# Kernel optimization log

Hardware: AMD Instinct MI355X
Metric: run time of the kernel (lower is better)

The kernel has to match this reference:

```python
import jax, jax.numpy as jnp
import numpy as np

NS, N_ATOMS = 16, 2000
NB, NA, NV, NT, NI = 2000, 4000, 400000, 6000, 1000
CHARGE = 18.222615


def setup_inputs() -> dict:
    key = jax.random.key(0)
    ks = jax.random.split(key, 24)
    u = lambda k, s: jax.random.uniform(k, s, dtype=jnp.float32)
    n = lambda k, s: jax.random.normal(k, s, dtype=jnp.float32)
    return {
        'length_bond': 1.0 + 0.5 * u(ks[0], (NS, NB)),
        'theta_angle': 1.5 + 0.5 * u(ks[1], (NS, NA)),
        'length_vdw': 3.0 + 5.0 * u(ks[2], (NS, NV)),
        'sin_cos_torsion': n(ks[3], (NS, NT, 8)),
        'cos2_imptors': u(ks[4], (NS, NI)),
        'vdw14': 0.5 + 0.5 * u(ks[5], (NV,)),
        'charge14': 0.5 + 0.5 * u(ks[6], (NV,)),
        'paras_bond': 0.5 + u(ks[7], (NB, 2)),
        'paras_angle': 0.5 + u(ks[8], (NA, 2)),
        'paras_vdw': 0.5 + u(ks[9], (N_ATOMS, 2)),
        'paras_charge': 0.3 * n(ks[10], (N_ATOMS,)),
        'paras_torsion': 0.5 * n(ks[11], (NT, 4)),
        'paras_imptors': 0.5 + u(ks[12], (NI, 1)),
        'dlength_bond': n(ks[13], (NS, NB, 6)),
        'dtheta_angle': n(ks[14], (NS, NA, 9)),
        'dlength_vdw': n(ks[15], (NS, NV, 6)),
        'dtheta_torsion': n(ks[16], (NS, NT, 12)),
        'dcos2_imptors': n(ks[17], (NS, NI, 12)),
        'nonbonded': jax.random.randint(ks[18], (2, NV), 0, N_ATOMS),
        'bond_index': jax.random.randint(ks[19], (NB, 2), 0, N_ATOMS),
        'angle_index': jax.random.randint(ks[20], (NA, 3), 0, N_ATOMS),
        'nonbonded_index': jax.random.randint(ks[21], (NV, 2), 0, N_ATOMS),
        'torsion_index': jax.random.randint(ks[22], (NT, 4), 0, N_ATOMS),
        'imptors_index': jax.random.randint(ks[23], (NI, 4), 0, N_ATOMS),
    }


def reference(length_bond, theta_angle, length_vdw, sin_cos_torsion, cos2_imptors,
              vdw14, charge14, paras_bond, paras_angle, paras_vdw, paras_charge,
              paras_torsion, paras_imptors, dlength_bond, dtheta_angle, dlength_vdw,
              dtheta_torsion, dcos2_imptors, nonbonded, bond_index, angle_index,
              nonbonded_index, torsion_index, imptors_index):
    ns = length_bond.shape[0]
    n_atoms = paras_vdw.shape[0]
    # --- bond (harmonic; bond_morse=False) ---
    K = paras_bond[:, 0] * 100.0
    r0 = paras_bond[:, 1]
    d = length_bond - r0[None]                      # (ns, NB)
    E_bond = K[None] * d * d
    F_bond = (dlength_bond * (2.0 * K)[None, :, None] * d[:, :, None]).reshape(ns, -1, 3)
    # --- angle ---
    Ka = paras_angle[:, 0] * 10.0
    th0 = paras_angle[:, 1] * (np.pi / 10.0)
    da = theta_angle - th0[None]
    E_angle = Ka[None] * da * da
    F_angle = (dtheta_angle * (2.0 * Ka)[None, :, None] * da[:, :, None]).reshape(ns, -1, 3)
    # --- Urey-Bradley disabled (bool_ub=False) ---
    E_ub = jnp.zeros((ns, 1), dtype=length_bond.dtype)
    # --- van der Waals (LJ-like) ---
    i, j = nonbonded[0], nonbonded[1]
    sigma = paras_vdw[i, 0] + paras_vdw[j, 0]       # (NV,)
    eps = (paras_vdw[i, 1] / 10.0) * (paras_vdw[j, 1] / 10.0) * vdw14
    t = (sigma[None] ** 6) / (length_vdw ** 6)      # (ns, NV)
    E_vdw = eps[None] * (t * t - 2.0 * t)
    F_vdw = (dlength_vdw * (12.0 * eps)[None, :, None]
             * (t * (1.0 - t) / length_vdw)[:, :, None]).reshape(ns, -1, 3)
    # --- Coulomb ---
    c1 = (CHARGE / 10.0) * paras_charge[i]
    c2 = (CHARGE / 10.0) * paras_charge[j]
    cc = (c1 * c2 * charge14)[None]                 # (1, NV)
    E_charge = cc / length_vdw
    F_charge = (-dlength_vdw * (cc / (length_vdw ** 2))[:, :, None]).reshape(ns, -1, 3)
    # --- torsion (cos at channels 1,3,5,7; sin at 0,2,4,6) ---
    cosn = sin_cos_torsion[:, :, 1::2]              # (ns, NT, 4)
    sinn = sin_cos_torsion[:, :, 0::2]
    E_torsion = jnp.einsum('stn,tn->st', cosn, paras_torsion)
    coeff = paras_torsion * jnp.arange(1, 5, dtype=paras_torsion.dtype)[None]
    F_torsion = (-dtheta_torsion * jnp.einsum('stn,tn->st', sinn, coeff)[:, :, None]).reshape(ns, -1, 3)
    # --- improper torsion ---
    ki = paras_imptors[:, 0]
    E_imptors = ki[None] * (1.0 - cos2_imptors)
    F_imptors = (-dcos2_imptors * ki[None, :, None]).reshape(ns, -1, 3)
    # --- scatter-add all force contributions into per-atom Force ---
    Force = jnp.zeros((ns, n_atoms, 3), dtype=length_bond.dtype)
    Force = Force.at[:, bond_index.reshape(-1)].add(F_bond)
    Force = Force.at[:, angle_index.reshape(-1)].add(F_angle)
    Force = Force.at[:, nonbonded_index.reshape(-1)].add(F_vdw)
    Force = Force.at[:, nonbonded_index.reshape(-1)].add(F_charge)
    Force = Force.at[:, torsion_index.reshape(-1)].add(F_torsion)
    Force = Force.at[:, imptors_index.reshape(-1)].add(F_imptors)
    # Pack Energy dict entries + Force into one (ns, total) array
    return jnp.concatenate([E_bond, E_angle, E_ub, E_vdw, E_charge,
                            E_torsion, E_imptors, Force.reshape(ns, -1)], axis=1)
```

## Files before the change

### kernel.cpp

```cpp
#include <hip/hip_runtime.h>
#include <hip/hip_fp16.h>

#define NS 16
#define N_ATOMS 2000
#define NB 2000
#define NA 4000
#define NV 400000
#define NT 6000
#define NI 1000

#define OUT_S 819001
#define OFF_EB 0
#define OFF_EA 2000
#define OFF_EUB 6000
#define OFF_EV 6001
#define OFF_EC 406001
#define OFF_ET 806001
#define OFF_EI 812001
#define OFF_F 813001

#define CHARGE_TENTH 1.8222615f

#define NBF 44000
#define BF_BOND 0
#define BF_ANGLE 4000
#define BF_TORS 16000
#define BF_IMP 40000
#define NENTV (NV * 2)
#define NBOND_TOT (NB + NA + NT + NI)
#define NITEMS (NV + NB + NA + NT + NI)
#define NCB 64
#define IPB ((NITEMS + NCB - 1) / NCB)
#define VBLKS ((NV + 255) / 256)
#define BBLKS ((NBOND_TOT + 255) / 256)

typedef float f2v __attribute__((ext_vector_type(2)));

__device__ __forceinline__ unsigned pkrtz(float a, float b) {
    typedef __fp16 hv2 __attribute__((ext_vector_type(2)));
    hv2 h = __builtin_amdgcn_cvt_pkrtz(a, b);
    return __builtin_bit_cast(unsigned, h);
}

__global__ __launch_bounds__(256, 4) void inithist_kernel(
    const float* __restrict__ v14, const float* __restrict__ q14,
    const float* __restrict__ pv, const float* __restrict__ pc,
    const int* __restrict__ nb,
    const int* __restrict__ nbi, const int* __restrict__ bidx,
    const int* __restrict__ aidx, const int* __restrict__ tidx,
    const int* __restrict__ iidx,
    float4* __restrict__ ws, int* __restrict__ countsV, int* __restrict__ countsB,
    float* __restrict__ out)
{
    __shared__ int hV[N_ATOMS];
    __shared__ int hB[N_ATOMS];
    int tid = threadIdx.x, b = blockIdx.x;

    if (b >= NCB) {
        int idx = (b - NCB) * 256 + tid;
        if (idx < NS) out[(size_t)idx * OUT_S + OFF_EUB] = 0.0f;
        if (idx < NV) {
            int v = idx;
            int i = nb[v];
            int j = nb[NV + v];
            float2 pvi = ((const float2*)pv)[i];
            float2 pvj = ((const float2*)pv)[j];
            float sigma = pvi.x + pvj.x;
            float sig2 = sigma * sigma;
            float4 w;
            w.x = sig2 * sig2 * sig2;
            w.y = pvi.y * pvj.y * 0.01f * v14[v];
            w.z = (CHARGE_TENTH * CHARGE_TENTH) * pc[i] * pc[j] * q14[v];
            w.w = 0.0f;
            ws[v] = w;
        }
        return;
    }

    for (int k = tid; k < N_ATOMS; k += 256) { hV[k] = 0; hB[k] = 0; }
    __syncthreads();
    int t0 = b * IPB, t1 = t0 + IPB; if (t1 > NITEMS) t1 = NITEMS;
    for (int t = t0 + tid; t < t1; t += 256) {
        if (t < NV) {
            atomicAdd(&hV[nbi[2 * t]], 1);
            atomicAdd(&hV[nbi[2 * t + 1]], 1);
        } else if (t < NV + NB) {
            int x = t - NV;
            atomicAdd(&hB[bidx[2 * x]], 1);
            atomicAdd(&hB[bidx[2 * x + 1]], 1);
        } else if (t < NV + NB + NA) {
            int x = t - (NV + NB);
            atomicAdd(&hB[aidx[3 * x]], 1);
            atomicAdd(&hB[aidx[3 * x + 1]], 1);
            atomicAdd(&hB[aidx[3 * x + 2]], 1);
        } else if (t < NV + NB + NA + NT) {
            int x = t - (NV + NB + NA);
            #pragma unroll
            for (int p = 0; p < 4; ++p) atomicAdd(&hB[tidx[4 * x + p]], 1);
        } else {
            int x = t - (NV + NB + NA + NT);
            #pragma unroll
            for (int p = 0; p < 4; ++p) atomicAdd(&hB[iidx[4 * x + p]], 1);
        }
    }
    __syncthreads();
    for (int k = tid; k < N_ATOMS; k += 256) {
        countsV[(size_t)b * N_ATOMS + k] = hV[k];
        countsB[(size_t)b * N_ATOMS + k] = hB[k];
    }
}

__global__ __launch_bounds__(256) void colscan2_kernel(
    int* __restrict__ countsV, int* __restrict__ countsB,
    int* __restrict__ totalV, int* __restrict__ totalB)
{
    int a = blockIdx.x * 256 + threadIdx.x;
    if (a < N_ATOMS) {
        int pre = 0;
        for (int b = 0; b < NCB; ++b) {
            int c = countsV[(size_t)b * N_ATOMS + a];
            countsV[(size_t)b * N_ATOMS + a] = pre;
            pre += c;
        }
        totalV[a] = pre;
    } else if (a < 2 * N_ATOMS) {
        int aa = a - N_ATOMS;
        int pre = 0;
        for (int b = 0; b < NCB; ++b) {
            int c = countsB[(size_t)b * N_ATOMS + aa];
            countsB[(size_t)b * N_ATOMS + aa] = pre;
            pre += c;
        }
        totalB[aa] = pre;
    }
}

__device__ __forceinline__ void wave_scan(const int* __restrict__ total,
                                          int* __restrict__ startx, int lane)
{
    const int CH = (N_ATOMS + 63) / 64;
    int a0 = lane * CH, a1 = a0 + CH; if (a1 > N_ATOMS) a1 = N_ATOMS;
    int tot = 0;
    for (int a = a0; a < a1; ++a) tot += total[a];
    int incl = tot;
    #pragma unroll
    for (int off = 1; off < 64; off <<= 1) {
        int n = __shfl_up(incl, off);
        if (lane >= off) incl += n;
    }
    int run = incl - tot;
    for (int a = a0; a < a1; ++a) { startx[a] = run; run += total[a]; }
    if (lane == 63) startx[N_ATOMS] = run;
}

__global__ __launch_bounds__(64) void scan2_kernel(
    const int* __restrict__ totalV, const int* __restrict__ totalB,
    int* __restrict__ startxV, int* __restrict__ startxB)
{
    int lane = threadIdx.x;
    wave_scan(totalV, startxV, lane);
    wave_scan(totalB, startxB, lane);
}

__global__ __launch_bounds__(256, 4) void place2_kernel(
    const int* __restrict__ nbi, const int* __restrict__ bidx,
    const int* __restrict__ aidx, const int* __restrict__ tidx,
    const int* __restrict__ iidx,
    const int* __restrict__ countsV, const int* __restrict__ countsB,
    const int* __restrict__ startxV, const int* __restrict__ startxB,
    int* __restrict__ posv, int* __restrict__ posb)
{
    __shared__ int curV[N_ATOMS];
    __shared__ int curB[N_ATOMS];
    int tid = threadIdx.x, b = blockIdx.x;
    for (int k = tid; k < N_ATOMS; k += 256) {
        curV[k] = startxV[k] + countsV[(size_t)b * N_ATOMS + k];
        curB[k] = startxB[k] + countsB[(size_t)b * N_ATOMS + k];
    }
    __syncthreads();
    int t0 = b * IPB, t1 = t0 + IPB; if (t1 > NITEMS) t1 = NITEMS;
    for (int t = t0 + tid; t < t1; t += 256) {
        if (t < NV) {
            posv[2 * t]     = atomicAdd(&curV[nbi[2 * t]], 1);
            posv[2 * t + 1] = atomicAdd(&curV[nbi[2 * t + 1]], 1);
        } else if (t < NV + NB) {
            int x = t - NV;
            #pragma unroll
            for (int sl = 0; sl < 2; ++sl)
                posb[BF_BOND + x * 2 + sl] = atomicAdd(&curB[bidx[2 * x + sl]], 1);
        } else if (t < NV + NB + NA) {
            int x = t - (NV + NB);
            #pragma unroll
            for (int sl = 0; sl < 3; ++sl)
                posb[BF_ANGLE + x * 3 + sl] = atomicAdd(&curB[aidx[3 * x + sl]], 1);
        } else if (t < NV + NB + NA + NT) {
            int x = t - (NV + NB + NA);
            #pragma unroll
            for (int sl = 0; sl < 4; ++sl)
                posb[BF_TORS + x * 4 + sl] = atomicAdd(&curB[tidx[4 * x + sl]], 1);
        } else {
            int x = t - (NV + NB + NA + NT);
            #pragma unroll
            for (int sl = 0; sl < 4; ++sl)
                posb[BF_IMP + x * 4 + sl] = atomicAdd(&curB[iidx[4 * x + sl]], 1);
        }
    }
}

__global__ __launch_bounds__(256, 2) void work_kernel(
    const float* __restrict__ lv, const float* __restrict__ dlv,
    const float4* __restrict__ ws, const int* __restrict__ posv,
    const float* __restrict__ lb, const float* __restrict__ th,
    const float* __restrict__ sc, const float* __restrict__ c2i,
    const float* __restrict__ pb, const float* __restrict__ pa,
    const float* __restrict__ pt, const float* __restrict__ pim,
    const float* __restrict__ dlb, const float* __restrict__ dth,
    const float* __restrict__ dtt, const float* __restrict__ dc2,
    const int* __restrict__ posb,
    unsigned* __restrict__ cV, unsigned* __restrict__ cB,
    float* __restrict__ out)
{
    int x = blockIdx.x;
    int tid = threadIdx.x;

    if (x < VBLKS) {
        int v = x * 256 + tid;
        if (v >= NV) return;
        float4 w = ws[v];
        int2 pp = *(const int2*)(posv + 2 * v);

        float2 dA[16], dB[16], dC[16];
        float rr[16];
        #pragma unroll
        for (int s = 0; s < 16; ++s) {
            const float2* p = (const float2*)(dlv + ((size_t)s * NV + v) * 6);
            dA[s] = p[0];
            dB[s] = p[1];
            dC[s] = p[2];
            rr[s] = lv[(size_t)s * NV + v];
        }
        __builtin_amdgcn_sched_barrier(0);

        unsigned cp[24];
        float hold[3][6];
        #pragma unroll
        for (int s = 0; s < 16; ++s) {
            float rinv = __builtin_amdgcn_rcpf(rr[s]);
            float r2inv = rinv * rinv;
            float r6inv = r2inv * r2inv * r2inv;
            float t = w.x * r6inv;
            out[(size_t)s * OUT_S + OFF_EV + v] = w.y * (t * t - 2.0f * t);
            out[(size_t)s * OUT_S + OFF_EC + v] = w.z * rinv;
            float fsv = 12.0f * w.y * t * (1.0f - t) * rinv - w.z * r2inv;
            float cc[6];
            cc[0] = dA[s].x * fsv; cc[1] = dA[s].y * fsv; cc[2] = dB[s].x * fsv;
            cc[3] = dB[s].y * fsv; cc[4] = dC[s].x * fsv; cc[5] = dC[s].y * fsv;
            int m = s & 3;
            if (m < 3) {
                #pragma unroll
                for (int k = 0; k < 6; ++k) hold[m][k] = cc[k];
            } else {
                int q = s >> 2;
                #pragma unroll
                for (int k = 0; k < 6; ++k) {
                    int t0 = __builtin_amdgcn_cvt_pk_fp8_f32(hold[0][k], hold[1][k], 0, false);
                    t0 = __builtin_amdgcn_cvt_pk_fp8_f32(hold[2][k], cc[k], t0, true);
                    cp[(k / 3) * 12 + (k % 3) * 4 + q] = (unsigned)t0;
                }
            }
        }
        uint4* dst0 = (uint4*)(cV + (size_t)pp.x * 12);
        #pragma unroll
        for (int k = 0; k < 3; ++k)
            dst0[k] = make_uint4(cp[4 * k], cp[4 * k + 1], cp[4 * k + 2], cp[4 * k + 3]);
        uint4* dst1 = (uint4*)(cV + (size_t)pp.y * 12);
        #pragma unroll
        for (int k = 0; k < 3; ++k)
            dst1[k] = make_uint4(cp[12 + 4 * k], cp[12 + 4 * k + 1], cp[12 + 4 * k + 2], cp[12 + 4 * k + 3]);
        return;
    }

    int t = (x - VBLKS) * 256 + tid;
    if (t >= NBOND_TOT) return;

    if (t < NB) {
        int b = t;
        float2 p = ((const float2*)pb)[b];
        float K = p.x * 100.0f;
        unsigned cp[48]; float hold[6];
        #pragma unroll
        for (int s = 0; s < 16; ++s) {
            float d = lb[s * NB + b] - p.y;
            out[(size_t)s * OUT_S + OFF_EB + b] = K * d * d;
            float g = 2.0f * K * d;
            const float2* dd = (const float2*)(dlb + ((size_t)s * NB + b) * 6);
            float2 dA = dd[0], dB = dd[1], dC = dd[2];
            float v0 = dA.x * g, v1 = dA.y * g, v2 = dB.x * g;
            float v3 = dB.y * g, v4 = dC.x * g, v5 = dC.y * g;
            if ((s & 1) == 0) { hold[0]=v0; hold[1]=v1; hold[2]=v2; hold[3]=v3; hold[4]=v4; hold[5]=v5; }
            else {
                int sp = s >> 1, h = sp >> 2, q = sp & 3;
                cp[0*24 + h*12 + 0*4 + q] = pkrtz(hold[0], v0);
                cp[0*24 + h*12 + 1*4 + q] = pkrtz(hold[1], v1);
                cp[0*24 + h*12 + 2*4 + q] = pkrtz(hold[2], v2);
                cp[1*24 + h*12 + 0*4 + q] = pkrtz(hold[3], v3);
                cp[1*24 + h*12 + 1*4 + q] = pkrtz(hold[4], v4);
                cp[1*24 + h*12 + 2*4 + q] = pkrtz(hold[5], v5);
            }
        }
        #pragma unroll
        for (int sl = 0; sl < 2; ++sl) {
            uint4* dst = (uint4*)(cB + (size_t)posb[BF_BOND + b * 2 + sl] * 24);
            #pragma unroll
            for (int k = 0; k < 6; ++k)
                dst[k] = make_uint4(cp[sl*24+4*k], cp[sl*24+4*k+1], cp[sl*24+4*k+2], cp[sl*24+4*k+3]);
        }
    } else if (t < NB + NA) {
        int a = t - NB;
        float2 p = ((const float2*)pa)[a];
        float Ka = p.x * 10.0f;
        float th0 = p.y * 0.31415926535f;
        unsigned cp[72]; float hold[9];
        #pragma unroll
        for (int s = 0; s < 16; ++s) {
            float da = th[s * NA + a] - th0;
            out[(size_t)s * OUT_S + OFF_EA + a] = Ka * da * da;
            float g = 2.0f * Ka * da;
            const float* dd = dth + ((size_t)s * NA + a) * 9;
            float v[9];
            #pragma unroll
            for (int k = 0; k < 9; ++k) v[k] = dd[k] * g;
            if ((s & 1) == 0) {
                #pragma unroll
                for (int k = 0; k < 9; ++k) hold[k] = v[k];
            } else {
                int sp = s >> 1, h = sp >> 2, q = sp & 3;
                #pragma unroll
                for (int k = 0; k < 9; ++k)
                    cp[(k / 3) * 24 + h * 12 + (k % 3) * 4 + q] = pkrtz(hold[k], v[k]);
            }
        }
        #pragma unroll
        for (int sl = 0; sl < 3; ++sl) {
            uint4* dst = (uint4*)(cB + (size_t)posb[BF_ANGLE + a * 3 + sl] * 24);
            #pragma unroll
            for (int k = 0; k < 6; ++k)
                dst[k] = make_uint4(cp[sl*24+4*k], cp[sl*24+4*k+1], cp[sl*24+4*k+2], cp[sl*24+4*k+3]);
        }
    } else if (t < NB + NA + NT) {
        int tt = t - (NB + NA);
        float4 p4 = ((const float4*)pt)[tt];
        unsigned cp[96]; float hold[12];
        #pragma unroll
        for (int s = 0; s < 16; ++s) {
            const float4* s8 = (const float4*)(sc + ((size_t)s * NT + tt) * 8);
            float4 sA = s8[0], sB = s8[1];
            out[(size_t)s * OUT_S + OFF_ET + tt] =
                sA.y * p4.x + sA.w * p4.y + sB.y * p4.z + sB.w * p4.w;
            float g = -(sA.x * p4.x + sA.z * p4.y * 2.0f + sB.x * p4.z * 3.0f + sB.z * p4.w * 4.0f);
            const float4* dd = (const float4*)(dtt + ((size_t)s * NT + tt) * 12);
            float4 dA = dd[0], dB = dd[1], dC = dd[2];
            float v[12] = {dA.x*g, dA.y*g, dA.z*g, dA.w*g, dB.x*g, dB.y*g,
                           dB.z*g, dB.w*g, dC.x*g, dC.y*g, dC.z*g, dC.w*g};
            if ((s & 1) == 0) {
                #pragma unroll
                for (int k = 0; k < 12; ++k) hold[k] = v[k];
            } else {
                int sp = s >> 1, h = sp >> 2, q = sp & 3;
                #pragma unroll
                for (int k = 0; k < 12; ++k)
                    cp[(k / 3) * 24 + h * 12 + (k % 3) * 4 + q] = pkrtz(hold[k], v[k]);
            }
        }
        #pragma unroll
        for (int sl = 0; sl < 4; ++sl) {
            uint4* dst = (uint4*)(cB + (size_t)posb[BF_TORS + tt * 4 + sl] * 24);
            #pragma unroll
            for (int k = 0; k < 6; ++k)
                dst[k] = make_uint4(cp[sl*24+4*k], cp[sl*24+4*k+1], cp[sl*24+4*k+2], cp[sl*24+4*k+3]);
        }
    } else {
        int ii = t - (NB + NA + NT);
        float ki = pim[ii];
        float g = -ki;
        unsigned cp[96]; float hold[12];
        #pragma unroll
        for (int s = 0; s < 16; ++s) {
            out[(size_t)s * OUT_S + OFF_EI + ii] = ki * (1.0f - c2i[s * NI + ii]);
            const float4* dd = (const float4*)(dc2 + ((size_t)s * NI + ii) * 12);
            float4 dA = dd[0], dB = dd[1], dC = dd[2];
            float v[12] = {dA.x*g, dA.y*g, dA.z*g, dA.w*g, dB.x*g, dB.y*g,
                           dB.z*g, dB.w*g, dC.x*g, dC.y*g, dC.z*g, dC.w*g};
            if ((s & 1) == 0) {
                #pragma unroll
                for (int k = 0; k < 12; ++k) hold[k] = v[k];
            } else {
                int sp = s >> 1, h = sp >> 2, q = sp & 3;
                #pragma unroll
                for (int k = 0; k < 12; ++k)
                    cp[(k / 3) * 24 + h * 12 + (k % 3) * 4 + q] = pkrtz(hold[k], v[k]);
            }
        }
        #pragma unroll
        for (int sl = 0; sl < 4; ++sl) {
            uint4* dst = (uint4*)(cB + (size_t)posb[BF_IMP + ii * 4 + sl] * 24);
            #pragma unroll
            for (int k = 0; k < 6; ++k)
                dst[k] = make_uint4(cp[sl*24+4*k], cp[sl*24+4*k+1], cp[sl*24+4*k+2], cp[sl*24+4*k+3]);
        }
    }
}

__global__ __launch_bounds__(256, 2) void gather2_kernel(
    const unsigned* __restrict__ cV, const unsigned* __restrict__ cB,
    const int* __restrict__ startxV, const int* __restrict__ startxB,
    float* __restrict__ out)
{
    __shared__ float red[4][48];
    int wv = threadIdx.x >> 6, lane = threadIdx.x & 63;
    int a0 = blockIdx.x * 4;
    int a = a0 + wv;

    float acc[48];
    #pragma unroll
    for (int k = 0; k < 48; ++k) acc[k] = 0.0f;

    {
        int base = startxV[a], endp = startxV[a + 1];
        for (int i = base + lane; i < endp; i += 64) {
            const uint4* e = (const uint4*)(cV + (size_t)i * 12);
            uint4 q0 = e[0], q1 = e[1], q2 = e[2];
            unsigned wd[12] = {q0.x, q0.y, q0.z, q0.w,
                               q1.x, q1.y, q1.z, q1.w,
                               q2.x, q2.y, q2.z, q2.w};
            #pragma unroll
            for (int wi = 0; wi < 12; ++wi) {
                int comp = wi >> 2, q = wi & 3;
                f2v lo = __builtin_amdgcn_cvt_pk_f32_fp8(wd[wi], false);
                f2v hi = __builtin_amdgcn_cvt_pk_f32_fp8(wd[wi], true);
                acc[comp * 16 + 4 * q + 0] += lo.x;
                acc[comp * 16 + 4 * q + 1] += lo.y;
                acc[comp * 16 + 4 * q + 2] += hi.x;
                acc[comp * 16 + 4 * q + 3] += hi.y;
            }
        }
    }
    {
        int base = startxB[a], endp = startxB[a + 1];
        for (int i = base + lane; i < endp; i += 64) {
            const uint4* e = (const uint4*)(cB + (size_t)i * 24);
            uint4 q0 = e[0], q1 = e[1], q2 = e[2], q3 = e[3], q4 = e[4], q5 = e[5];
            unsigned wd[24] = {q0.x, q0.y, q0.z, q0.w, q1.x, q1.y, q1.z, q1.w,
                               q2.x, q2.y, q2.z, q2.w, q3.x, q3.y, q3.z, q3.w,
                               q4.x, q4.y, q4.z, q4.w, q5.x, q5.y, q5.z, q5.w};
            #pragma unroll
            for (int wi = 0; wi < 24; ++wi) {
                int h = wi / 12, rem = wi - h * 12;
                int comp = rem >> 2, qq = rem & 3;
                int s0 = h * 8 + 2 * qq;
                __half2 hh = __builtin_bit_cast(__half2, wd[wi]);
                acc[comp * 16 + s0]     += __low2float(hh);
                acc[comp * 16 + s0 + 1] += __high2float(hh);
            }
        }
    }

    #pragma unroll
    for (int off = 32; off > 0; off >>= 1) {
        #pragma unroll
        for (int k = 0; k < 48; ++k)
            acc[k] += __shfl_down(acc[k], off);
    }
    if (lane == 0) {
        #pragma unroll
        for (int k = 0; k < 48; ++k) red[wv][k] = acc[k];
    }
    __syncthreads();
    int th = threadIdx.x;
    if (th < 192) {
        int s = th / 12, idx = th % 12;
        int ai = idx / 3, comp = idx % 3;
        out[(size_t)s * OUT_S + OFF_F + 3 * (a0 + ai) + comp] = red[ai][comp * 16 + s];
    }
}

extern "C" void kernel_launch(void* const* d_in, const int* in_sizes, int n_in,
                              void* d_out, int out_size, void* d_ws, size_t ws_size,
                              hipStream_t stream) {
    const float* lb  = (const float*)d_in[0];
    const float* th  = (const float*)d_in[1];
    const float* lv  = (const float*)d_in[2];
    const float* sc  = (const float*)d_in[3];
    const float* c2i = (const float*)d_in[4];
    const float* v14 = (const float*)d_in[5];
    const float* q14 = (const float*)d_in[6];
    const float* pb  = (const float*)d_in[7];
    const float* pa  = (const float*)d_in[8];
    const float* pv  = (const float*)d_in[9];
    const float* pc  = (const float*)d_in[10];
    const float* pt  = (const float*)d_in[11];
    const float* pim = (const float*)d_in[12];
    const float* dlb = (const float*)d_in[13];
    const float* dth = (const float*)d_in[14];
    const float* dlv = (const float*)d_in[15];
    const float* dtt = (const float*)d_in[16];
    const float* dc2 = (const float*)d_in[17];
    const int* nb    = (const int*)d_in[18];
    const int* bidx  = (const int*)d_in[19];
    const int* aidx  = (const int*)d_in[20];
    const int* nbi   = (const int*)d_in[21];
    const int* tidx  = (const int*)d_in[22];
    const int* iidx  = (const int*)d_in[23];
    float* out = (float*)d_out;

    unsigned* cV      = (unsigned*)d_ws;
    unsigned* cB      = cV + (size_t)NENTV * 12;
    float4*   wsp     = (float4*)(cB + (size_t)NBF * 24);
    int*      posv    = (int*)(wsp + NV);
    int*      posb    = posv + 2 * NV;
    int*      countsV = posb + NBF;
    int*      countsB = countsV + (size_t)NCB * N_ATOMS;
    int*      totalV  = countsB + (size_t)NCB * N_ATOMS;
    int*      totalB  = totalV + N_ATOMS;
    int*      startxV = totalB + N_ATOMS;
    int*      startxB = startxV + (N_ATOMS + 1);

    inithist_kernel<<<NCB + VBLKS, 256, 0, stream>>>(
        v14, q14, pv, pc, nb, nbi, bidx, aidx, tidx, iidx,
        wsp, countsV, countsB, out);
    colscan2_kernel<<<(2 * N_ATOMS + 255) / 256, 256, 0, stream>>>(countsV, countsB, totalV, totalB);
    scan2_kernel<<<1, 64, 0, stream>>>(totalV, totalB, startxV, startxB);
    place2_kernel<<<NCB, 256, 0, stream>>>(nbi, bidx, aidx, tidx, iidx,
                                           countsV, countsB, startxV, startxB, posv, posb);
    work_kernel<<<VBLKS + BBLKS, 256, 0, stream>>>(
        lv, dlv, wsp, posv, lb, th, sc, c2i, pb, pa, pt, pim,
        dlb, dth, dtt, dc2, posb, cV, cB, out);
    gather2_kernel<<<N_ATOMS / 4, 256, 0, stream>>>(cV, cB, startxV, startxB, out);
}
```

Measured before the change: 157.4 us.

## Split bonded work across two threads per term and reorder block schedule

Bonded-term threads now each handle half of the 16 samples, which doubles thread count for the bonded section and halves per-thread register arrays. Bonded blocks are moved ahead of the vdw blocks so the long-running bonded tail starts first. The vdw path stops prefetching all 16 samples into registers and loads per iteration instead, and launch bounds raise the occupancy target from 2 to 4 blocks per CU. This lowers register pressure and trades explicit load batching for higher occupancy.

```diff
diff --git a/kernel.cpp b/kernel.cpp
--- a/kernel.cpp
+++ b/kernel.cpp
@@ -32,7 +32,7 @@
 #define NCB 64
 #define IPB ((NITEMS + NCB - 1) / NCB)
 #define VBLKS ((NV + 255) / 256)
-#define BBLKS ((NBOND_TOT + 255) / 256)
+#define BBH ((NBOND_TOT * 2 + 255) / 256)
 
 typedef float f2v __attribute__((ext_vector_type(2)));
 
@@ -207,7 +207,7 @@
     }
 }
 
-__global__ __launch_bounds__(256, 2) void work_kernel(
+__global__ __launch_bounds__(256, 4) void work_kernel(
     const float* __restrict__ lv, const float* __restrict__ dlv,
     const float4* __restrict__ ws, const int* __restrict__ posv,
     const float* __restrict__ lb, const float* __restrict__ th,
@@ -223,29 +223,19 @@
     int x = blockIdx.x;
     int tid = threadIdx.x;
 
-    if (x < VBLKS) {
-        int v = x * 256 + tid;
+    if (x >= BBH) {
+        int v = (x - BBH) * 256 + tid;
         if (v >= NV) return;
         float4 w = ws[v];
         int2 pp = *(const int2*)(posv + 2 * v);
-
-        float2 dA[16], dB[16], dC[16];
-        float rr[16];
-        #pragma unroll
-        for (int s = 0; s < 16; ++s) {
-            const float2* p = (const float2*)(dlv + ((size_t)s * NV + v) * 6);
-            dA[s] = p[0];
-            dB[s] = p[1];
-            dC[s] = p[2];
-            rr[s] = lv[(size_t)s * NV + v];
-        }
-        __builtin_amdgcn_sched_barrier(0);
-
         unsigned cp[24];
         float hold[3][6];
         #pragma unroll
         for (int s = 0; s < 16; ++s) {
-            float rinv = __builtin_amdgcn_rcpf(rr[s]);
+            float r = lv[(size_t)s * NV + v];
+            const float2* d2 = (const float2*)(dlv + ((size_t)s * NV + v) * 6);
+            float2 dA = d2[0], dB = d2[1], dC = d2[2];
+            float rinv = __builtin_amdgcn_rcpf(r);
             float r2inv = rinv * rinv;
             float r6inv = r2inv * r2inv * r2inv;
             float t = w.x * r6inv;
@@ -253,8 +243,8 @@
             out[(size_t)s * OUT_S + OFF_EC + v] = w.z * rinv;
             float fsv = 12.0f * w.y * t * (1.0f - t) * rinv - w.z * r2inv;
             float cc[6];
-            cc[0] = dA[s].x * fsv; cc[1] = dA[s].y * fsv; cc[2] = dB[s].x * fsv;
-            cc[3] = dB[s].y * fsv; cc[4] = dC[s].x * fsv; cc[5] = dC[s].y * fsv;
+            cc[0] = dA.x * fsv; cc[1] = dA.y * fsv; cc[2] = dB.x * fsv;
+            cc[3] = dB.y * fsv; cc[4] = dC.x * fsv; cc[5] = dC.y * fsv;
             int m = s & 3;
             if (m < 3) {
                 #pragma unroll
@@ -280,16 +270,20 @@
         return;
     }
 
-    int t = (x - VBLKS) * 256 + tid;
+    int idx = x * 256 + tid;
+    int h = idx & 1;
+    int t = idx >> 1;
     if (t >= NBOND_TOT) return;
+    int sbase = h * 8;
 
     if (t < NB) {
         int b = t;
         float2 p = ((const float2*)pb)[b];
         float K = p.x * 100.0f;
-        unsigned cp[48]; float hold[6];
-        #pragma unroll
-        for (int s = 0; s < 16; ++s) {
+        unsigned cp[24]; float hold[6];
+        #pragma unroll
+        for (int j = 0; j < 8; ++j) {
+            int s = sbase + j;
             float d = lb[s * NB + b] - p.y;
             out[(size_t)s * OUT_S + OFF_EB + b] = K * d * d;
             float g = 2.0f * K * d;
@@ -297,32 +291,33 @@
             float2 dA = dd[0], dB = dd[1], dC = dd[2];
             float v0 = dA.x * g, v1 = dA.y * g, v2 = dB.x * g;
             float v3 = dB.y * g, v4 = dC.x * g, v5 = dC.y * g;
-            if ((s & 1) == 0) { hold[0]=v0; hold[1]=v1; hold[2]=v2; hold[3]=v3; hold[4]=v4; hold[5]=v5; }
+            if ((j & 1) == 0) { hold[0]=v0; hold[1]=v1; hold[2]=v2; hold[3]=v3; hold[4]=v4; hold[5]=v5; }
             else {
-                int sp = s >> 1, h = sp >> 2, q = sp & 3;
-                cp[0*24 + h*12 + 0*4 + q] = pkrtz(hold[0], v0);
-                cp[0*24 + h*12 + 1*4 + q] = pkrtz(hold[1], v1);
-                cp[0*24 + h*12 + 2*4 + q] = pkrtz(hold[2], v2);
-                cp[1*24 + h*12 + 0*4 + q] = pkrtz(hold[3], v3);
-                cp[1*24 + h*12 + 1*4 + q] = pkrtz(hold[4], v4);
-                cp[1*24 + h*12 + 2*4 + q] = pkrtz(hold[5], v5);
+                int q = j >> 1;
+                cp[0*12 + 0*4 + q] = pkrtz(hold[0], v0);
+                cp[0*12 + 1*4 + q] = pkrtz(hold[1], v1);
+                cp[0*12 + 2*4 + q] = pkrtz(hold[2], v2);
+                cp[1*12 + 0*4 + q] = pkrtz(hold[3], v3);
+                cp[1*12 + 1*4 + q] = pkrtz(hold[4], v4);
+                cp[1*12 + 2*4 + q] = pkrtz(hold[5], v5);
             }
         }
         #pragma unroll
         for (int sl = 0; sl < 2; ++sl) {
-            uint4* dst = (uint4*)(cB + (size_t)posb[BF_BOND + b * 2 + sl] * 24);
-            #pragma unroll
-            for (int k = 0; k < 6; ++k)
-                dst[k] = make_uint4(cp[sl*24+4*k], cp[sl*24+4*k+1], cp[sl*24+4*k+2], cp[sl*24+4*k+3]);
+            uint4* dst = (uint4*)(cB + (size_t)posb[BF_BOND + b * 2 + sl] * 24 + h * 12);
+            #pragma unroll
+            for (int k = 0; k < 3; ++k)
+                dst[k] = make_uint4(cp[sl*12+4*k], cp[sl*12+4*k+1], cp[sl*12+4*k+2], cp[sl*12+4*k+3]);
         }
     } else if (t < NB + NA) {
         int a = t - NB;
         float2 p = ((const float2*)pa)[a];
         float Ka = p.x * 10.0f;
         float th0 = p.y * 0.31415926535f;
-        unsigned cp[72]; float hold[9];
-        #pragma unroll
-        for (int s = 0; s < 16; ++s) {
+        unsigned cp[36]; float hold[9];
+        #pragma unroll
+        for (int j = 0; j < 8; ++j) {
+            int s = sbase + j;
             float da = th[s * NA + a] - th0;
             out[(size_t)s * OUT_S + OFF_EA + a] = Ka * da * da;
             float g = 2.0f * Ka * da;
@@ -330,29 +325,30 @@
             float v[9];
             #pragma unroll
             for (int k = 0; k < 9; ++k) v[k] = dd[k] * g;
-            if ((s & 1) == 0) {
+            if ((j & 1) == 0) {
                 #pragma unroll
                 for (int k = 0; k < 9; ++k) hold[k] = v[k];
             } else {
-                int sp = s >> 1, h = sp >> 2, q = sp & 3;
+                int q = j >> 1;
                 #pragma unroll
                 for (int k = 0; k < 9; ++k)
-                    cp[(k / 3) * 24 + h * 12 + (k % 3) * 4 + q] = pkrtz(hold[k], v[k]);
+                    cp[(k / 3) * 12 + (k % 3) * 4 + q] = pkrtz(hold[k], v[k]);
             }
         }
         #pragma unroll
         for (int sl = 0; sl < 3; ++sl) {
-            uint4* dst = (uint4*)(cB + (size_t)posb[BF_ANGLE + a * 3 + sl] * 24);
-            #pragma unroll
-            for (int k = 0; k < 6; ++k)
-                dst[k] = make_uint4(cp[sl*24+4*k], cp[sl*24+4*k+1], cp[sl*24+4*k+2], cp[sl*24+4*k+3]);
+            uint4* dst = (uint4*)(cB + (size_t)posb[BF_ANGLE + a * 3 + sl] * 24 + h * 12);
+            #pragma unroll
+            for (int k = 0; k < 3; ++k)
+                dst[k] = make_uint4(cp[sl*12+4*k], cp[sl*12+4*k+1], cp[sl*12+4*k+2], cp[sl*12+4*k+3]);
         }
     } else if (t < NB + NA + NT) {
         int tt = t - (NB + NA);
         float4 p4 = ((const float4*)pt)[tt];
-        unsigned cp[96]; float hold[12];
-        #pragma unroll
-        for (int s = 0; s < 16; ++s) {
+        unsigned cp[48]; float hold[12];
+        #pragma unroll
+        for (int j = 0; j < 8; ++j) {
+            int s = sbase + j;
             const float4* s8 = (const float4*)(sc + ((size_t)s * NT + tt) * 8);
             float4 sA = s8[0], sB = s8[1];
             out[(size_t)s * OUT_S + OFF_ET + tt] =
@@ -362,51 +358,52 @@
             float4 dA = dd[0], dB = dd[1], dC = dd[2];
             float v[12] = {dA.x*g, dA.y*g, dA.z*g, dA.w*g, dB.x*g, dB.y*g,
                            dB.z*g, dB.w*g, dC.x*g, dC.y*g, dC.z*g, dC.w*g};
-            if ((s & 1) == 0) {
+            if ((j & 1) == 0) {
                 #pragma unroll
                 for (int k = 0; k < 12; ++k) hold[k] = v[k];
             } else {
-                int sp = s >> 1, h = sp >> 2, q = sp & 3;
+                int q = j >> 1;
                 #pragma unroll
                 for (int k = 0; k < 12; ++k)
-                    cp[(k / 3) * 24 + h * 12 + (k % 3) * 4 + q] = pkrtz(hold[k], v[k]);
+                    cp[(k / 3) * 12 + (k % 3) * 4 + q] = pkrtz(hold[k], v[k]);
             }
         }
         #pragma unroll
         for (int sl = 0; sl < 4; ++sl) {
-            uint4* dst = (uint4*)(cB + (size_t)posb[BF_TORS + tt * 4 + sl] * 24);
-            #pragma unroll
-            for (int k = 0; k < 6; ++k)
-                dst[k] = make_uint4(cp[sl*24+4*k], cp[sl*24+4*k+1], cp[sl*24+4*k+2], cp[sl*24+4*k+3]);
+            uint4* dst = (uint4*)(cB + (size_t)posb[BF_TORS + tt * 4 + sl] * 24 + h * 12);
+            #pragma unroll
+            for (int k = 0; k < 3; ++k)
+                dst[k] = make_uint4(cp[sl*12+4*k], cp[sl*12+4*k+1], cp[sl*12+4*k+2], cp[sl*12+4*k+3]);
         }
     } else {
         int ii = t - (NB + NA + NT);
         float ki = pim[ii];
         float g = -ki;
-        unsigned cp[96]; float hold[12];
-        #pragma unroll
-        for (int s = 0; s < 16; ++s) {
+        unsigned cp[48]; float hold[12];
+        #pragma unroll
+        for (int j = 0; j < 8; ++j) {
+            int s = sbase + j;
             out[(size_t)s * OUT_S + OFF_EI + ii] = ki * (1.0f - c2i[s * NI + ii]);
             const float4* dd = (const float4*)(dc2 + ((size_t)s * NI + ii) * 12);
             float4 dA = dd[0], dB = dd[1], dC = dd[2];
             float v[12] = {dA.x*g, dA.y*g, dA.z*g, dA.w*g, dB.x*g, dB.y*g,
                            dB.z*g, dB.w*g, dC.x*g, dC.y*g, dC.z*g, dC.w*g};
-            if ((s & 1) == 0) {
+            if ((j & 1) == 0) {
                 #pragma unroll
                 for (int k = 0; k < 12; ++k) hold[k] = v[k];
             } else {
-                int sp = s >> 1, h = sp >> 2, q = sp & 3;
+                int q = j >> 1;
                 #pragma unroll
                 for (int k = 0; k < 12; ++k)
-                    cp[(k / 3) * 24 + h * 12 + (k % 3) * 4 + q] = pkrtz(hold[k], v[k]);
+                    cp[(k / 3) * 12 + (k % 3) * 4 + q] = pkrtz(hold[k], v[k]);
             }
         }
         #pragma unroll
         for (int sl = 0; sl < 4; ++sl) {
-            uint4* dst = (uint4*)(cB + (size_t)posb[BF_IMP + ii * 4 + sl] * 24);
-            #pragma unroll
-            for (int k = 0; k < 6; ++k)
-                dst[k] = make_uint4(cp[sl*24+4*k], cp[sl*24+4*k+1], cp[sl*24+4*k+2], cp[sl*24+4*k+3]);
+            uint4* dst = (uint4*)(cB + (size_t)posb[BF_IMP + ii * 4 + sl] * 24 + h * 12);
+            #pragma unroll
+            for (int k = 0; k < 3; ++k)
+                dst[k] = make_uint4(cp[sl*12+4*k], cp[sl*12+4*k+1], cp[sl*12+4*k+2], cp[sl*12+4*k+3]);
         }
     }
 }
@@ -532,7 +529,7 @@
     scan2_kernel<<<1, 64, 0, stream>>>(totalV, totalB, startxV, startxB);
     place2_kernel<<<NCB, 256, 0, stream>>>(nbi, bidx, aidx, tidx, iidx,
                                            countsV, countsB, startxV, startxB, posv, posb);
-    work_kernel<<<VBLKS + BBLKS, 256, 0, stream>>>(
+    work_kernel<<<BBH + VBLKS, 256, 0, stream>>>(
         lv, dlv, wsp, posv, lb, th, sc, c2i, pb, pa, pt, pim,
         dlb, dth, dtt, dc2, posb, cV, cB, out);
     gather2_kernel<<<N_ATOMS / 4, 256, 0, stream>>>(cV, cB, startxV, startxB, out);
```

New measurement: 140.7 us. -10.6%, faster.
